# Kernel optimization log

Hardware: AMD Instinct MI355X
Metric: run time of the kernel (lower is better)

Reference implementation:

```python
import jax, jax.numpy as jnp
from jax import lax
import numpy as np

NPOINT = 1024
NSAMPLE = 32
BN_EPS = 1e-3  # Keras BatchNormalization default epsilon


def farthest_point_sample(xyz, npoint):
    # xyz: [B, N, 3] -> indices [B, npoint] (int32), sequential O(npoint*N)
    B, N, _ = xyz.shape

    def step(carry, _):
        distance, farthest = carry                                   # [B,N], [B]
        centroid = jnp.take_along_axis(xyz, farthest[:, None, None], axis=1)  # [B,1,3]
        dist = jnp.sum((xyz - centroid) ** 2, axis=-1)               # [B,N]
        distance = jnp.minimum(distance, dist)
        new_farthest = jnp.argmax(distance, axis=1).astype(jnp.int32)
        return (distance, new_farthest), farthest

    init = (jnp.full((B, N), 1e10, xyz.dtype), jnp.zeros((B,), jnp.int32))
    _, idxs = lax.scan(step, init, xs=None, length=npoint)           # [npoint, B]
    return jnp.transpose(idxs)                                       # [B, npoint]


def index_points_2d(points, idx):
    # points: [B,N,C], idx: [B,S] -> [B,S,C]
    return jnp.take_along_axis(points, idx[:, :, None], axis=1)


def index_points_3d(points, idx):
    # points: [B,N,C], idx: [B,S,K] -> [B,S,K,C]
    return jax.vmap(lambda p, i: p[i])(points, idx)


def query_ball_point(nsample, xyz, new_xyz):
    # nearest-nsample variant (radius is ignored, matching the source)
    # sq_dist: [B, S, N]
    sq = jnp.sum(new_xyz ** 2, axis=-1, keepdims=True) \
         - 2.0 * jnp.einsum('bsc,bnc->bsn', new_xyz, xyz) \
         + jnp.sum(xyz ** 2, axis=-1)[:, None, :]
    _, group_idx = lax.top_k(-sq, nsample)                           # [B,S,K]
    return group_idx


def bn_relu(x, g, b, mm, mv):
    # inference-mode BatchNorm (moving stats) + ReLU, per-channel on last dim
    return jax.nn.relu((x - mm) * lax.rsqrt(mv + BN_EPS) * g + b)


def setup_inputs() -> dict:
    key = jax.random.key(0)
    ks = jax.random.split(key, 20)
    B, N, D = 4, 16384, 64
    mlp = [64, 64, 128]
    cin = 3 + D  # 67
    inp = {
        'xyz': jax.random.normal(ks[0], (B, N, 3), jnp.float32),
        'points': jax.random.normal(ks[1], (B, N, D), jnp.float32),
    }
    c = cin
    for i, co in enumerate(mlp):
        inp[f'w{i}'] = jax.random.normal(ks[2 + 4 * i], (c, co), jnp.float32) * (1.0 / np.sqrt(c))
        inp[f'g{i}'] = jnp.ones((co,), jnp.float32)
        inp[f'b{i}'] = jnp.zeros((co,), jnp.float32)
        inp[f'mm{i}'] = jax.random.normal(ks[3 + 4 * i], (co,), jnp.float32) * 0.1
        inp[f'mv{i}'] = jax.random.uniform(ks[4 + 4 * i], (co,), jnp.float32, 0.5, 1.5)
        c = co
    return inp


def reference(xyz, points, w0, g0, b0, mm0, mv0, w1, g1, b1, mm1, mv1, w2, g2, b2, mm2, mv2):
    fps_idx = farthest_point_sample(xyz, NPOINT)                     # [B,S]
    new_xyz = index_points_2d(xyz, fps_idx)                          # [B,S,3]
    idx = query_ball_point(NSAMPLE, xyz, new_xyz)                    # [B,S,K]
    grouped_xyz = index_points_3d(xyz, idx)                          # [B,S,K,3]
    grouped_xyz_norm = grouped_xyz - new_xyz[:, :, None, :]
    grouped_points = index_points_3d(points, idx)                    # [B,S,K,D]
    x = jnp.concatenate([grouped_xyz_norm, grouped_points], axis=-1) # [B,S,K,3+D]
    for w, g, b, mm, mv in ((w0, g0, b0, mm0, mv0), (w1, g1, b1, mm1, mv1), (w2, g2, b2, mm2, mv2)):
        x = bn_relu(jnp.einsum('bskc,co->bsko', x, w), g, b, mm, mv)
    new_points = jnp.max(x, axis=2)                                  # [B,S,C_out]
    return (new_xyz, new_points)
```

## Files before the change

### kernel.cpp

```cpp
#include <hip/hip_runtime.h>
#include <hip/hip_bf16.h>
#include <stdint.h>

#define N_PTS 16384
#define S_OUT 1024


typedef float v2f __attribute__((ext_vector_type(2)));

__global__ __launch_bounds__(512)
__attribute__((amdgpu_waves_per_eu(2, 2)))
void fps_kernel(
    const float* __restrict__ xyz,
    float* __restrict__ out_newxyz)
{
#pragma clang fp contract(off)
  const int b    = blockIdx.x;
  const int tid  = threadIdx.x;
  const int lane = tid & 63;
  const int wid  = tid >> 6;
  const float* base = xyz + (size_t)b * N_PTS * 3;

  v2f px[16], py[16], pz[16], dist[16];
#pragma unroll
  for (int i = 0; i < 16; ++i) {
    int n0 = (tid * 32 + 2 * i) * 3;
    px[i] = (v2f){ base[n0 + 0], base[n0 + 3] };
    py[i] = (v2f){ base[n0 + 1], base[n0 + 4] };
    pz[i] = (v2f){ base[n0 + 2], base[n0 + 5] };
    dist[i] = (v2f){ 1e10f, 1e10f };
  }

  __shared__ unsigned long long sred[2][8];

  float cx = base[0], cy = base[1], cz = base[2];

  for (int s = 0; s < S_OUT; ++s) {
    if (tid == 0) {
      size_t o = ((size_t)b * S_OUT + s) * 3;
      out_newxyz[o + 0] = cx;
      out_newxyz[o + 1] = cy;
      out_newxyz[o + 2] = cz;
    }
    if (s == S_OUT - 1) break;

    const v2f cx2 = (v2f){ cx, cx };
    const v2f cy2 = (v2f){ cy, cy };
    const v2f cz2 = (v2f){ cz, cz };

    float m0 = -1.0f, m1 = -1.0f, m2 = -1.0f, m3 = -1.0f;
#pragma unroll
    for (int i = 0; i < 16; ++i) {
      v2f dx = px[i] - cx2;
      v2f dy = py[i] - cy2;
      v2f dz = pz[i] - cz2;
      v2f dd = (dx * dx + dy * dy) + dz * dz;
      v2f dm = __builtin_elementwise_min(dist[i], dd);
      dist[i] = dm;
      if ((i & 3) == 0)      m0 = fmaxf(fmaxf(m0, dm.x), dm.y);
      else if ((i & 3) == 1) m1 = fmaxf(fmaxf(m1, dm.x), dm.y);
      else if ((i & 3) == 2) m2 = fmaxf(fmaxf(m2, dm.x), dm.y);
      else                   m3 = fmaxf(fmaxf(m3, dm.x), dm.y);
    }
    const float lm = fmaxf(fmaxf(m0, m1), fmaxf(m2, m3));

    float wm = lm;
#pragma unroll
    for (int off = 1; off < 64; off <<= 1)
      wm = fmaxf(wm, __shfl_xor(wm, off));

    unsigned bestN = 0;
    if (lm == wm) {
      unsigned msk = 0u;
#pragma unroll
      for (int i = 0; i < 16; ++i) {
        msk |= (dist[i].x == wm) ? (1u << (2 * i))     : 0u;
        msk |= (dist[i].y == wm) ? (1u << (2 * i + 1)) : 0u;
      }
      bestN = (unsigned)(tid * 32) + (unsigned)(__ffs(msk) - 1);
    }
    unsigned long long wmask = __ballot(lm == wm);
    int wl = __ffsll(wmask) - 1;
    unsigned wn = (unsigned)__shfl((int)bestN, wl);

    const int p = s & 1;
    if (lane == 0)
      sred[p][wid] = ((unsigned long long)__float_as_uint(wm) << 32) |
                     (unsigned long long)(0xFFFFFFFFu - wn);
    __syncthreads();

    unsigned long long k = sred[p][lane & 7];
#pragma unroll
    for (int off = 1; off < 8; off <<= 1) {
      unsigned long long o = __shfl_xor(k, off);
      if (o > k) k = o;
    }
    unsigned n = 0xFFFFFFFFu - (unsigned)(k & 0xFFFFFFFFull);
    n = __builtin_amdgcn_readfirstlane(n);
    const float* pc = base + (size_t)n * 3;
    cx = pc[0]; cy = pc[1]; cz = pc[2];
  }
}

__global__ __launch_bounds__(256, 2) void knn_kernel(
    const float* __restrict__ xyz,
    const float* __restrict__ newxyz,
    int* __restrict__ knn_out)
{
  const int bs  = blockIdx.x;
  const int b   = bs >> 10;
  const int tid = threadIdx.x;
  const float* base = xyz + (size_t)b * N_PTS * 3;

  const float qx = newxyz[(size_t)bs * 3 + 0];
  const float qy = newxyz[(size_t)bs * 3 + 1];
  const float qz = newxyz[(size_t)bs * 3 + 2];
  const float sumq = __fadd_rn(__fadd_rn(__fmul_rn(qx, qx), __fmul_rn(qy, qy)),
                               __fmul_rn(qz, qz));

  __shared__ unsigned hist[2048];
  __shared__ unsigned tsum[256];
  __shared__ unsigned long long cand[512];
  __shared__ unsigned long long s_min;
  __shared__ int s_b1, s_r1, s_b2, s_r2, s_cntL, s_cntC;

  for (int i = tid; i < 2048; i += 256) hist[i] = 0;
  if (tid == 0) { s_cntL = 0; s_cntC = 0; }
  __syncthreads();

#define KNN_KEY(n, u)                                                          \
    float x = base[(n) * 3 + 0];                                               \
    float y = base[(n) * 3 + 1];                                               \
    float z = base[(n) * 3 + 2];                                               \
    float sumx = __fadd_rn(__fadd_rn(__fmul_rn(x, x), __fmul_rn(y, y)),        \
                           __fmul_rn(z, z));                                   \
    float dot  = __fmul_rn(qx, x);                                             \
    dot = fmaf(qy, y, dot);                                                    \
    dot = fmaf(qz, z, dot);                                                    \
    float sq   = __fsub_rn(__fadd_rn(sumq, sumx), __fmul_rn(2.0f, dot));       \
    unsigned u = __float_as_uint(sq);                                          \
    u ^= (u & 0x80000000u) ? 0xFFFFFFFFu : 0x80000000u;

  for (int j = 0; j < 64; ++j) {
    int n = j * 256 + tid;
    KNN_KEY(n, u)
    atomicAdd(&hist[u >> 21], 1u);
  }
  __syncthreads();

  unsigned ts = 0;
#pragma unroll
  for (int u = 0; u < 8; ++u) ts += hist[tid * 8 + u];
  tsum[tid] = ts;
  __syncthreads();

  if (tid == 0) {
    unsigned acc = 0; int t2 = 0;
    for (; t2 < 256; ++t2) { unsigned h = tsum[t2]; if (acc + h >= 32u) break; acc += h; }
    int u2 = t2 * 8;
    for (;; ++u2) { unsigned h = hist[u2]; if (acc + h >= 32u) break; acc += h; }
    s_b1 = u2; s_r1 = 32 - (int)acc;
  }
  __syncthreads();
  const unsigned b1 = (unsigned)s_b1;
  const int r1 = s_r1;

  for (int i = tid; i < 2048; i += 256) hist[i] = 0;
  __syncthreads();

  for (int j = 0; j < 64; ++j) {
    int n = j * 256 + tid;
    KNN_KEY(n, u)
    if ((u >> 21) == b1) atomicAdd(&hist[(u >> 10) & 0x7FFu], 1u);
  }
  __syncthreads();

  ts = 0;
#pragma unroll
  for (int u = 0; u < 8; ++u) ts += hist[tid * 8 + u];
  tsum[tid] = ts;
  __syncthreads();

  if (tid == 0) {
    unsigned acc = 0; int t2 = 0;
    for (; t2 < 256; ++t2) { unsigned h = tsum[t2]; if (acc + h >= (unsigned)r1) break; acc += h; }
    int u2 = t2 * 8;
    for (;; ++u2) { unsigned h = hist[u2]; if (acc + h >= (unsigned)r1) break; acc += h; }
    s_b2 = u2; s_r2 = r1 - (int)acc;
  }
  __syncthreads();
  const unsigned b2 = (unsigned)s_b2;

  int* outp = knn_out + (size_t)bs * 32;

  for (int j = 0; j < 64; ++j) {
    int n = j * 256 + tid;
    KNN_KEY(n, u)
    unsigned bin = u >> 21;
    if (bin < b1) {
      int p = atomicAdd(&s_cntL, 1);
      outp[p] = n;
    } else if (bin == b1) {
      unsigned sub = (u >> 10) & 0x7FFu;
      if (sub < b2) {
        int p = atomicAdd(&s_cntL, 1);
        outp[p] = n;
      } else if (sub == b2) {
        int p = atomicAdd(&s_cntC, 1);
        if (p < 512) cand[p] = ((unsigned long long)u << 32) | (unsigned)n;
      }
    }
  }
  __syncthreads();
#undef KNN_KEY

  const int r   = s_r2;
  const int cl  = s_cntL;
  const int cnt = min(s_cntC, 512);
  unsigned long long last = 0ull;
  for (int i = 0; i < r; ++i) {
    if (tid == 0) s_min = ~0ull;
    __syncthreads();
    for (int p = tid; p < cnt; p += 256) {
      unsigned long long v = cand[p];
      if (i == 0 ? 1 : (v > last)) atomicMin(&s_min, v);
    }
    __syncthreads();
    unsigned long long m = s_min;
    if (tid == 0) outp[cl + i] = (int)(unsigned)(m & 0xFFFFFFFFull);
    last = m;
    __syncthreads();
  }
}

__global__ __launch_bounds__(256, 2) void mlp_kernel(
    const float* __restrict__ xyz,
    const float* __restrict__ points,
    const float* __restrict__ newxyz,
    const int* __restrict__ knn,
    const float* __restrict__ w0, const float* __restrict__ g0,
    const float* __restrict__ b0, const float* __restrict__ mm0,
    const float* __restrict__ mv0,
    const float* __restrict__ w1, const float* __restrict__ g1,
    const float* __restrict__ b1_, const float* __restrict__ mm1,
    const float* __restrict__ mv1,
    const float* __restrict__ w2, const float* __restrict__ g2,
    const float* __restrict__ b2_, const float* __restrict__ mm2,
    const float* __restrict__ mv2,
    float* __restrict__ out1)
{
  const int tid = threadIdx.x;
  const int BS0 = blockIdx.x * 2;

  __shared__ __align__(16) float xT[2][67][36];
  __shared__ __align__(16) float a1[2][64][36];
  __shared__ __align__(16) float wbuf[8192];

  {
    const int sg = tid >> 7;
    const int j  = (tid >> 2) & 31;
    const int cq = tid & 3;
    const int S  = BS0 + sg;
    const int bb = S >> 10;
    const int n  = knn[(size_t)S * 32 + j] & (N_PTS - 1);
    const float* pbase = points + ((size_t)bb * N_PTS + n) * 64;
    const float* xbase = xyz + ((size_t)bb * N_PTS + n) * 3;
    for (int c = cq; c < 67; c += 4) {
      float v;
      if (c < 3) v = __fsub_rn(xbase[c], newxyz[(size_t)S * 3 + c]);
      else       v = pbase[c - 3];
      xT[sg][c][j] = v;
    }
  }
  for (int i = tid; i < 67 * 64; i += 256) wbuf[i] = w0[i];
  __syncthreads();

  const int sg = tid >> 7;
  const int t  = tid & 127;

  {
    const int ot = t & 15, kt = t >> 4;
    const int o0 = ot * 4, k0 = kt * 4;
    float acc[4][4] = {};
    for (int c = 0; c < 67; ++c) {
      float4 xv = *(const float4*)&xT[sg][c][k0];
      float4 wq = *(const float4*)&wbuf[c * 64 + o0];
      float wv[4] = { wq.x, wq.y, wq.z, wq.w };
      float xs[4] = { xv.x, xv.y, xv.z, xv.w };
#pragma unroll
      for (int a = 0; a < 4; ++a)
#pragma unroll
        for (int k2 = 0; k2 < 4; ++k2)
          acc[a][k2] = fmaf(wv[a], xs[k2], acc[a][k2]);
    }
#pragma unroll
    for (int jj = 0; jj < 4; ++jj) {
      int o = o0 + jj;
      float A  = rsqrtf(mv0[o] + 1e-3f) * g0[o];
      float Bc = b0[o] - mm0[o] * A;
      float4 y;
      y.x = fmaxf(fmaf(acc[jj][0], A, Bc), 0.0f);
      y.y = fmaxf(fmaf(acc[jj][1], A, Bc), 0.0f);
      y.z = fmaxf(fmaf(acc[jj][2], A, Bc), 0.0f);
      y.w = fmaxf(fmaf(acc[jj][3], A, Bc), 0.0f);
      *(float4*)&a1[sg][o][k0] = y;
    }
  }
  __syncthreads();
  for (int i = tid; i < 64 * 64; i += 256) wbuf[i] = w1[i];
  __syncthreads();

  {
    const int ot = t & 15, kt = t >> 4;
    const int o0 = ot * 4, k0 = kt * 4;
    float acc[4][4] = {};
    for (int c = 0; c < 64; ++c) {
      float4 xv = *(const float4*)&a1[sg][c][k0];
      float4 wq = *(const float4*)&wbuf[c * 64 + o0];
      float wv[4] = { wq.x, wq.y, wq.z, wq.w };
      float xs[4] = { xv.x, xv.y, xv.z, xv.w };
#pragma unroll
      for (int a = 0; a < 4; ++a)
#pragma unroll
        for (int k2 = 0; k2 < 4; ++k2)
          acc[a][k2] = fmaf(wv[a], xs[k2], acc[a][k2]);
    }
#pragma unroll
    for (int jj = 0; jj < 4; ++jj) {
      int o = o0 + jj;
      float A  = rsqrtf(mv1[o] + 1e-3f) * g1[o];
      float Bc = b1_[o] - mm1[o] * A;
      float4 y;
      y.x = fmaxf(fmaf(acc[jj][0], A, Bc), 0.0f);
      y.y = fmaxf(fmaf(acc[jj][1], A, Bc), 0.0f);
      y.z = fmaxf(fmaf(acc[jj][2], A, Bc), 0.0f);
      y.w = fmaxf(fmaf(acc[jj][3], A, Bc), 0.0f);
      *(float4*)&xT[sg][o][k0] = y;
    }
  }
  __syncthreads();
  for (int i = tid; i < 64 * 128; i += 256) wbuf[i] = w2[i];
  __syncthreads();

  float* pm = &a1[0][0][0];
  {
    const int ot = t & 31, kt = t >> 5;
    const int o0 = ot * 4, k0 = kt * 8;
    float acc[4][8] = {};
    for (int c = 0; c < 64; ++c) {
      float4 xa = *(const float4*)&xT[sg][c][k0];
      float4 xb = *(const float4*)&xT[sg][c][k0 + 4];
      float4 wq = *(const float4*)&wbuf[c * 128 + o0];
      float wv[4] = { wq.x, wq.y, wq.z, wq.w };
      float xs[8] = { xa.x, xa.y, xa.z, xa.w, xb.x, xb.y, xb.z, xb.w };
#pragma unroll
      for (int a = 0; a < 4; ++a)
#pragma unroll
        for (int k2 = 0; k2 < 8; ++k2)
          acc[a][k2] = fmaf(wv[a], xs[k2], acc[a][k2]);
    }
#pragma unroll
    for (int jj = 0; jj < 4; ++jj) {
      int o = o0 + jj;
      float A  = rsqrtf(mv2[o] + 1e-3f) * g2[o];
      float Bc = b2_[o] - mm2[o] * A;
      float m = 0.0f;
#pragma unroll
      for (int kk = 0; kk < 8; ++kk)
        m = fmaxf(m, fmaf(acc[jj][kk], A, Bc));
      pm[((sg * 128 + o) << 2) + kt] = m;
    }
  }
  __syncthreads();
  {
    const int sg2 = tid >> 7, o = tid & 127;
    const int basep = (sg2 * 128 + o) << 2;
    float m = fmaxf(fmaxf(pm[basep + 0], pm[basep + 1]),
                    fmaxf(pm[basep + 2], pm[basep + 3]));
    out1[(size_t)(BS0 + sg2) * 128 + o] = m;
  }
}

extern "C" void kernel_launch(void* const* d_in, const int* in_sizes, int n_in,
                              void* d_out, int out_size, void* d_ws, size_t ws_size,
                              hipStream_t stream) {
  const float* xyz    = (const float*)d_in[0];
  const float* points = (const float*)d_in[1];
  const float* w0  = (const float*)d_in[2];
  const float* g0  = (const float*)d_in[3];
  const float* b0  = (const float*)d_in[4];
  const float* mm0 = (const float*)d_in[5];
  const float* mv0 = (const float*)d_in[6];
  const float* w1  = (const float*)d_in[7];
  const float* g1  = (const float*)d_in[8];
  const float* b1  = (const float*)d_in[9];
  const float* mm1 = (const float*)d_in[10];
  const float* mv1 = (const float*)d_in[11];
  const float* w2  = (const float*)d_in[12];
  const float* g2  = (const float*)d_in[13];
  const float* b2  = (const float*)d_in[14];
  const float* mm2 = (const float*)d_in[15];
  const float* mv2 = (const float*)d_in[16];

  float* out      = (float*)d_out;
  float* out_pts  = out + (size_t)4 * 1024 * 3;
  int*   knn      = (int*)d_ws;

  fps_kernel<<<4, 512, 0, stream>>>(xyz, out);
  knn_kernel<<<4096, 256, 0, stream>>>(xyz, out, knn);
  mlp_kernel<<<2048, 256, 0, stream>>>(xyz, points, out, knn,
      w0, g0, b0, mm0, mv0, w1, g1, b1, mm1, mv1, w2, g2, b2, mm2, mv2,
      out_pts);
}
```

Baseline: 2.440 ms.

## Restructure FPS argmax: float-only reduction, winner wave fetches centroid from registers

The per-iteration argmax in farthest point sampling now reduces only float maxima across waves through shared memory instead of packed 64-bit value/index keys. Only the winning wave resolves the index, selecting the centroid coordinates from its register-resident points with a select tree and publishing them through shared memory. This removes the 64-bit shuffle reduction and the dependent global load of the centroid from the serial critical path. In exchange it adds a second barrier per iteration plus extra select work in one wave.

After: 2.640 ms. 8.2% more time.

```diff
diff --git a/kernel.cpp b/kernel.cpp
--- a/kernel.cpp
+++ b/kernel.cpp
@@ -31,7 +31,8 @@
     dist[i] = (v2f){ 1e10f, 1e10f };
   }
 
-  __shared__ unsigned long long sred[2][8];
+  __shared__ float swred[8];
+  __shared__ float s_cent[3];
 
   float cx = base[0], cy = base[1], cz = base[2];
 
@@ -48,7 +49,7 @@
     const v2f cy2 = (v2f){ cy, cy };
     const v2f cz2 = (v2f){ cz, cz };
 
-    float m0 = -1.0f, m1 = -1.0f, m2 = -1.0f, m3 = -1.0f;
+    v2f b0 = (v2f){ -1.0f, -1.0f }, b1 = (v2f){ -1.0f, -1.0f };
 #pragma unroll
     for (int i = 0; i < 16; ++i) {
       v2f dx = px[i] - cx2;
@@ -57,48 +58,80 @@
       v2f dd = (dx * dx + dy * dy) + dz * dz;
       v2f dm = __builtin_elementwise_min(dist[i], dd);
       dist[i] = dm;
-      if ((i & 3) == 0)      m0 = fmaxf(fmaxf(m0, dm.x), dm.y);
-      else if ((i & 3) == 1) m1 = fmaxf(fmaxf(m1, dm.x), dm.y);
-      else if ((i & 3) == 2) m2 = fmaxf(fmaxf(m2, dm.x), dm.y);
-      else                   m3 = fmaxf(fmaxf(m3, dm.x), dm.y);
-    }
-    const float lm = fmaxf(fmaxf(m0, m1), fmaxf(m2, m3));
+      if (i & 1) b1 = __builtin_elementwise_max(b1, dm);
+      else       b0 = __builtin_elementwise_max(b0, dm);
+    }
+    v2f bm = __builtin_elementwise_max(b0, b1);
+    const float lm = fmaxf(bm.x, bm.y);
 
     float wm = lm;
 #pragma unroll
     for (int off = 1; off < 64; off <<= 1)
       wm = fmaxf(wm, __shfl_xor(wm, off));
-
-    unsigned bestN = 0;
-    if (lm == wm) {
+    if (lane == 0) swred[wid] = wm;
+    __syncthreads();
+
+    float s0 = swred[0], s1 = swred[1], s2 = swred[2], s3 = swred[3];
+    float s4 = swred[4], s5 = swred[5], s6 = swred[6], s7 = swred[7];
+    float M = fmaxf(fmaxf(fmaxf(s0, s1), fmaxf(s2, s3)),
+                    fmaxf(fmaxf(s4, s5), fmaxf(s6, s7)));
+    int wf = 7;
+    wf = (s6 == M) ? 6 : wf;
+    wf = (s5 == M) ? 5 : wf;
+    wf = (s4 == M) ? 4 : wf;
+    wf = (s3 == M) ? 3 : wf;
+    wf = (s2 == M) ? 2 : wf;
+    wf = (s1 == M) ? 1 : wf;
+    wf = (s0 == M) ? 0 : wf;
+
+    if (wid == wf) {
+      unsigned long long bal = __ballot(lm == M);
+      int ll = __ffsll(bal) - 1;
       unsigned msk = 0u;
 #pragma unroll
       for (int i = 0; i < 16; ++i) {
-        msk |= (dist[i].x == wm) ? (1u << (2 * i))     : 0u;
-        msk |= (dist[i].y == wm) ? (1u << (2 * i + 1)) : 0u;
-      }
-      bestN = (unsigned)(tid * 32) + (unsigned)(__ffs(msk) - 1);
-    }
-    unsigned long long wmask = __ballot(lm == wm);
-    int wl = __ffsll(wmask) - 1;
-    unsigned wn = (unsigned)__shfl((int)bestN, wl);
-
-    const int p = s & 1;
-    if (lane == 0)
-      sred[p][wid] = ((unsigned long long)__float_as_uint(wm) << 32) |
-                     (unsigned long long)(0xFFFFFFFFu - wn);
+        msk |= (dist[i].x == M) ? (1u << (2 * i)) : 0u;
+        msk |= (dist[i].y == M) ? (1u << (2 * i + 1)) : 0u;
+      }
+      int bi = __ffs(msk) - 1;
+      int pi = (bi >> 1) & 15;
+      v2f x8[8], y8[8], z8[8];
+#pragma unroll
+      for (int j = 0; j < 8; ++j) {
+        bool c = (pi & 1);
+        x8[j] = c ? px[2 * j + 1] : px[2 * j];
+        y8[j] = c ? py[2 * j + 1] : py[2 * j];
+        z8[j] = c ? pz[2 * j + 1] : pz[2 * j];
+      }
+      v2f x4[4], y4[4], z4[4];
+#pragma unroll
+      for (int j = 0; j < 4; ++j) {
+        bool c = ((pi >> 1) & 1);
+        x4[j] = c ? x8[2 * j + 1] : x8[2 * j];
+        y4[j] = c ? y8[2 * j + 1] : y8[2 * j];
+        z4[j] = c ? z8[2 * j + 1] : z8[2 * j];
+      }
+      v2f x2[2], y2[2], z2[2];
+#pragma unroll
+      for (int j = 0; j < 2; ++j) {
+        bool c = ((pi >> 2) & 1);
+        x2[j] = c ? x4[2 * j + 1] : x4[2 * j];
+        y2[j] = c ? y4[2 * j + 1] : y4[2 * j];
+        z2[j] = c ? z4[2 * j + 1] : z4[2 * j];
+      }
+      bool c3 = ((pi >> 3) & 1);
+      v2f xf = c3 ? x2[1] : x2[0];
+      v2f yf = c3 ? y2[1] : y2[0];
+      v2f zf = c3 ? z2[1] : z2[0];
+      bool cs = (bi & 1);
+      if (lane == ll) {
+        s_cent[0] = cs ? xf.y : xf.x;
+        s_cent[1] = cs ? yf.y : yf.x;
+        s_cent[2] = cs ? zf.y : zf.x;
+      }
+    }
     __syncthreads();
-
-    unsigned long long k = sred[p][lane & 7];
-#pragma unroll
-    for (int off = 1; off < 8; off <<= 1) {
-      unsigned long long o = __shfl_xor(k, off);
-      if (o > k) k = o;
-    }
-    unsigned n = 0xFFFFFFFFu - (unsigned)(k & 0xFFFFFFFFull);
-    n = __builtin_amdgcn_readfirstlane(n);
-    const float* pc = base + (size_t)n * 3;
-    cx = pc[0]; cy = pc[1]; cz = pc[2];
+    cx = s_cent[0]; cy = s_cent[1]; cz = s_cent[2];
   }
 }
 
```
